# Kernel optimization log

Measured on AMD Instinct MI355X. Metric: run time of the kernel, lower is better.

The kernel has to match this reference:

```python
import jax, jax.numpy as jnp
import numpy as np

N_PTS = 262144
N_GAUSS = 2048
NZ, NY, NX = 100, 100, 100
MAX_SCALE = 0.02
BG = -1.0
CUTOFF = 9.0  # 3-sigma Mahalanobis cutoff
CHUNK = 1024


def quat_to_rot(q):
    # q: [G,4] normalized quaternion (r, x, y, z) as in 3DGS
    r, x, y, z = q[:, 0], q[:, 1], q[:, 2], q[:, 3]
    R = jnp.stack([
        1 - 2 * (y * y + z * z), 2 * (x * y - r * z), 2 * (x * z + r * y),
        2 * (x * y + r * z), 1 - 2 * (x * x + z * z), 2 * (y * z - r * x),
        2 * (x * z - r * y), 2 * (y * z + r * x), 1 - 2 * (x * x + y * y),
    ], axis=-1)
    return R.reshape(-1, 3, 3)


def setup_inputs() -> dict:
    key = jax.random.key(0)
    k = jax.random.split(key, 7)
    x = jax.random.uniform(k[0], (N_PTS, 3), jnp.float32, -1.0, 1.0)
    xyz = jax.random.uniform(k[1], (N_GAUSS, 3), jnp.float32)
    # raw log-scales so exp(raw) ~ 0.01 (Gaussians a few cells wide)
    scaling_raw = jax.random.normal(k[2], (N_GAUSS, 3), jnp.float32) * 0.3 + jnp.log(0.01)
    rotation_raw = jax.random.normal(k[3], (N_GAUSS, 4), jnp.float32)
    weight_raw = jax.random.normal(k[4], (N_GAUSS, 1), jnp.float32)
    values_raw = jax.random.normal(k[5], (N_GAUSS, 1), jnp.float32)
    valid_grid = jax.random.uniform(k[6], (NZ * NY * NX,)) < 0.8
    return {"x": x, "xyz": xyz, "scaling_raw": scaling_raw,
            "rotation_raw": rotation_raw, "weight_raw": weight_raw,
            "values_raw": values_raw, "valid_grid": valid_grid}


def _forward(x, xyz, scaling_raw, rotation_raw, weight_raw, values_raw, valid_grid):
    # valid-mask lookup from nearest grid cell
    x01 = (x + 1.0) * 0.5
    ix = jnp.clip(jnp.round(x01[:, 0] * (NX - 1)).astype(jnp.int32), 0, NX - 1)
    iy = jnp.clip(jnp.round(x01[:, 1] * (NY - 1)).astype(jnp.int32), 0, NY - 1)
    iz = jnp.clip(jnp.round(x01[:, 2] * (NZ - 1)).astype(jnp.int32), 0, NZ - 1)
    flat_idx = iz * (NY * NX) + iy * NX + ix
    valid = valid_grid[flat_idx]
    # world coords: mesh normalized to [0,1]^3 so vol_min=0, extent=1
    xw = x01
    # activations on Gaussian parameters
    s = jnp.exp(scaling_raw)
    r = jnp.linalg.norm(s, axis=1, keepdims=True) + 1e-8
    r_soft = MAX_SCALE * jnp.tanh(r / MAX_SCALE)
    s = s * (r_soft / r)                           # capped scales [G,3]
    qn = rotation_raw / jnp.maximum(
        jnp.linalg.norm(rotation_raw, axis=1, keepdims=True), 1e-12)
    R = quat_to_rot(qn)                            # [G,3,3]
    inv_s2 = 1.0 / (s * s)
    A = jnp.einsum('gik,gk,gjk->gij', R, inv_s2, R)  # inverse covariance [G,3,3]
    w = jax.nn.sigmoid(weight_raw[:, 0])           # [G]
    v = jax.nn.sigmoid(values_raw[:, 0])           # [G]
    wv = w * v
    xs = xw.reshape(-1, CHUNK, 3)                  # scan over point chunks

    def step(_, xc):
        d = xc[:, None, :] - xyz[None, :, :]       # [C,G,3]
        qd = jnp.einsum('cgi,gij,cgj->cg', d, A, d)
        g = jnp.where(qd <= CUTOFF, jnp.exp(-0.5 * qd), 0.0)  # [C,G]
        den = g @ w
        num = g @ wv
        y = jnp.where(den > 0, num / jnp.where(den > 0, den, 1.0), BG)
        return None, y

    _, ys = jax.lax.scan(step, None, xs)
    y = jnp.where(valid, ys.reshape(-1), 0.0)
    return y.reshape(-1, 1)


def reference(x, xyz, scaling_raw, rotation_raw, weight_raw, values_raw, valid_grid):
    return _forward(x, xyz, scaling_raw, rotation_raw, weight_raw, values_raw, valid_grid)
```

## Files before the change

kernel.cpp:

```cpp
#include <hip/hip_runtime.h>
#include <hip/hip_bf16.h>

namespace {

constexpr int GRIDC = 16;
constexpr int NCELL = GRIDC * GRIDC * GRIDC;
constexpr int CAP   = 48;
constexpr int RECF  = 16;
constexpr int PREPB = 8;
constexpr int CPB   = NCELL / PREPB;

__device__ __forceinline__ float sigmoid_(float v) {
    if (v >= 0.0f) { float e = expf(-v); return 1.0f / (1.0f + e); }
    float e = expf(v); return e / (1.0f + e);
}

__global__ void __launch_bounds__(256)
VEG_setup(const unsigned char* __restrict__ vg,
          const float* __restrict__ xyz, const float* __restrict__ sraw,
          const float* __restrict__ rraw, const float* __restrict__ wraw,
          const float* __restrict__ vraw,
          float* __restrict__ recs, int* __restrict__ counts,
          int* __restrict__ mode_p, int ng) {
    __shared__ int scount[CPB];
    __shared__ int sf1, sf3;
    if (threadIdx.x == 0) { sf1 = 0; sf3 = 0; }
    for (int c = threadIdx.x; c < CPB; c += 256) scount[c] = 0;
    __syncthreads();

    if (blockIdx.x == 0) {
        uint4 v = ((const uint4*)vg)[threadIdx.x];
        unsigned m = v.x | v.y | v.z | v.w;
        if (m & 0x0000FF00u) atomicOr(&sf1, 1);
        if (m & 0xFF000000u) atomicOr(&sf3, 1);
    }

    int cellbase = blockIdx.x * CPB;
    for (int g = threadIdx.x; g < ng; g += 256) {
        float s0 = expf(sraw[g * 3 + 0]);
        float s1 = expf(sraw[g * 3 + 1]);
        float s2 = expf(sraw[g * 3 + 2]);
        float r  = sqrtf(s0 * s0 + s1 * s1 + s2 * s2) + 1e-8f;
        float rs = 0.02f * tanhf(r / 0.02f);
        float fsc = rs / r;
        s0 *= fsc; s1 *= fsc; s2 *= fsc;

        float rad = 3.0f * fmaxf(fmaxf(s0, s1), s2);
        rad = rad * 1.001f + 1e-6f;
        float cx = xyz[g * 3 + 0], cy = xyz[g * 3 + 1], cz = xyz[g * 3 + 2];

        int xlo = max(0, (int)floorf((cx - rad) * (float)GRIDC));
        int xhi = min(GRIDC - 1, (int)floorf((cx + rad) * (float)GRIDC));
        int ylo = max(0, (int)floorf((cy - rad) * (float)GRIDC));
        int yhi = min(GRIDC - 1, (int)floorf((cy + rad) * (float)GRIDC));
        int zlo = max(0, (int)floorf((cz - rad) * (float)GRIDC));
        int zhi = min(GRIDC - 1, (int)floorf((cz + rad) * (float)GRIDC));
        int cmin = (zlo * GRIDC + ylo) * GRIDC + xlo;
        int cmax = (zhi * GRIDC + yhi) * GRIDC + xhi;
        if (cmax < cellbase || cmin >= cellbase + CPB) continue;

        float q0 = rraw[g * 4 + 0], q1 = rraw[g * 4 + 1];
        float q2 = rraw[g * 4 + 2], q3 = rraw[g * 4 + 3];
        float qn = fmaxf(sqrtf(q0 * q0 + q1 * q1 + q2 * q2 + q3 * q3), 1e-12f);
        float inv = 1.0f / qn;
        float rr = q0 * inv, qx = q1 * inv, qy = q2 * inv, qz = q3 * inv;
        float R00 = 1.0f - 2.0f * (qy * qy + qz * qz);
        float R01 = 2.0f * (qx * qy - rr * qz);
        float R02 = 2.0f * (qx * qz + rr * qy);
        float R10 = 2.0f * (qx * qy + rr * qz);
        float R11 = 1.0f - 2.0f * (qx * qx + qz * qz);
        float R12 = 2.0f * (qy * qz - rr * qx);
        float R20 = 2.0f * (qx * qz - rr * qy);
        float R21 = 2.0f * (qy * qz + rr * qx);
        float R22 = 1.0f - 2.0f * (qx * qx + qy * qy);

        float i0 = 1.0f / (s0 * s0), i1 = 1.0f / (s1 * s1), i2 = 1.0f / (s2 * s2);
        float4 rA = make_float4(cx, cy, cz,
                                R00 * R00 * i0 + R01 * R01 * i1 + R02 * R02 * i2);
        float4 rB = make_float4(R10 * R10 * i0 + R11 * R11 * i1 + R12 * R12 * i2,
                                R20 * R20 * i0 + R21 * R21 * i1 + R22 * R22 * i2,
                                R00 * R10 * i0 + R01 * R11 * i1 + R02 * R12 * i2,
                                R00 * R20 * i0 + R01 * R21 * i1 + R02 * R22 * i2);
        float w = sigmoid_(wraw[g]);
        float v = sigmoid_(vraw[g]);
        float4 rC = make_float4(R10 * R20 * i0 + R11 * R21 * i1 + R12 * R22 * i2,
                                w, w * v, 0.0f);

        for (int zz = zlo; zz <= zhi; ++zz)
            for (int yy = ylo; yy <= yhi; ++yy)
                for (int xx = xlo; xx <= xhi; ++xx) {
                    int cell  = (zz * GRIDC + yy) * GRIDC + xx;
                    int local = cell - cellbase;
                    if ((unsigned)local < (unsigned)CPB) {
                        int slot = atomicAdd(&scount[local], 1);
                        if (slot < CAP) {
                            float4* o = (float4*)(recs +
                                        ((size_t)cell * CAP + slot) * RECF);
                            o[0] = rA; o[1] = rB; o[2] = rC;
                        }
                    }
                }
    }
    __syncthreads();
    for (int c = threadIdx.x; c < CPB; c += 256) counts[cellbase + c] = scount[c];
    if (blockIdx.x == 0 && threadIdx.x == 0) *mode_p = sf1 ? 0 : (sf3 ? 2 : 1);
}

__global__ void __launch_bounds__(256)
VEG_splat(const float* __restrict__ x, const float* __restrict__ recs,
          const int* __restrict__ counts,
          const void* __restrict__ valid, const int* __restrict__ mode_p,
          float* __restrict__ out, int npts) {
    __shared__ float shx[768];
    int base = blockIdx.x * 256;
    int nrem = npts - base;
    if (nrem >= 256) {
        if (threadIdx.x < 192)
            ((float4*)shx)[threadIdx.x] = ((const float4*)(x + (size_t)base * 3))[threadIdx.x];
    } else {
        for (int j = threadIdx.x; j < nrem * 3; j += 256)
            shx[j] = x[(size_t)base * 3 + j];
    }
    __syncthreads();

    int i = base + threadIdx.x;
    if (i >= npts) return;

    float px = (shx[threadIdx.x * 3 + 0] + 1.0f) * 0.5f;
    float py = (shx[threadIdx.x * 3 + 1] + 1.0f) * 0.5f;
    float pz = (shx[threadIdx.x * 3 + 2] + 1.0f) * 0.5f;

    int cx = min(GRIDC - 1, (int)(px * (float)GRIDC));
    int cy = min(GRIDC - 1, (int)(py * (float)GRIDC));
    int cz = min(GRIDC - 1, (int)(pz * (float)GRIDC));
    int cell = (cz * GRIDC + cy) * GRIDC + cx;
    int cnt = counts[cell];
    const float4* rec = (const float4*)(recs + (size_t)cell * CAP * RECF);

    int ix = min(99, max(0, (int)rintf(px * 99.0f)));
    int iy = min(99, max(0, (int)rintf(py * 99.0f)));
    int iz = min(99, max(0, (int)rintf(pz * 99.0f)));
    int flat = iz * 10000 + iy * 100 + ix;

    int mode = *mode_p;
    bool vb;
    if (mode == 0)      vb = ((const unsigned char*)valid)[flat] != 0;
    else if (mode == 1) vb = ((const int*)valid)[flat] != 0;
    else                vb = ((const float*)valid)[flat] != 0.0f;

    cnt = (cnt < 0) ? 0 : min(cnt, CAP);
    float den = 0.0f, num = 0.0f;
#pragma unroll 2
    for (int j = 0; j < cnt; ++j) {
        float4 A = rec[j * 4 + 0], B = rec[j * 4 + 1], C = rec[j * 4 + 2];
        float dx = px - A.x, dy = py - A.y, dz = pz - A.z;
        float qd = A.w * dx * dx + B.x * dy * dy + B.y * dz * dz +
                   2.0f * (B.z * dx * dy + B.w * dx * dz + C.x * dy * dz);
        if (qd <= 9.0f) {
            float e = __expf(-0.5f * qd);
            den = fmaf(C.y, e, den);
            num = fmaf(C.z, e, num);
        }
    }
    float y = (den > 0.0f) ? (num / den) : -1.0f;
    out[i] = vb ? y : 0.0f;
}

__global__ void VEG_detect(const unsigned char* vg, int* mode) {
    __shared__ int f1, f3;
    if (threadIdx.x == 0) { f1 = 0; f3 = 0; }
    __syncthreads();
    for (int i = threadIdx.x; i < 4096; i += blockDim.x) {
        unsigned char b = vg[i];
        if (b) {
            int m = i & 3;
            if (m == 1) atomicOr(&f1, 1);
            if (m == 3) atomicOr(&f3, 1);
        }
    }
    __syncthreads();
    if (threadIdx.x == 0) *mode = f1 ? 0 : (f3 ? 2 : 1);
}

__global__ void __launch_bounds__(256)
VEG_brute(const float* __restrict__ x, const float* __restrict__ xyz,
          const float* __restrict__ sraw, const float* __restrict__ rraw,
          const float* __restrict__ wraw, const float* __restrict__ vraw,
          const void* __restrict__ valid, const int* __restrict__ mode_p,
          float* __restrict__ out, int npts, int ng) {
    __shared__ float sh[256 * 12];
    int i = blockIdx.x * blockDim.x + threadIdx.x;
    bool inb = i < npts;
    float px = 0, py = 0, pz = 0; int flat = 0;
    if (inb) {
        px = (x[i * 3 + 0] + 1.0f) * 0.5f;
        py = (x[i * 3 + 1] + 1.0f) * 0.5f;
        pz = (x[i * 3 + 2] + 1.0f) * 0.5f;
        int ix = min(99, max(0, (int)rintf(px * 99.0f)));
        int iy = min(99, max(0, (int)rintf(py * 99.0f)));
        int iz = min(99, max(0, (int)rintf(pz * 99.0f)));
        flat = iz * 10000 + iy * 100 + ix;
    }
    float den = 0.0f, num = 0.0f;
    for (int base = 0; base < ng; base += 256) {
        __syncthreads();
        int g = base + threadIdx.x;
        if (g < ng) {
            float s0 = expf(sraw[g * 3 + 0]);
            float s1 = expf(sraw[g * 3 + 1]);
            float s2 = expf(sraw[g * 3 + 2]);
            float r  = sqrtf(s0 * s0 + s1 * s1 + s2 * s2) + 1e-8f;
            float rs = 0.02f * tanhf(r / 0.02f);
            float fsc = rs / r;
            s0 *= fsc; s1 *= fsc; s2 *= fsc;
            float q0 = rraw[g * 4 + 0], q1 = rraw[g * 4 + 1];
            float q2 = rraw[g * 4 + 2], q3 = rraw[g * 4 + 3];
            float qn = fmaxf(sqrtf(q0 * q0 + q1 * q1 + q2 * q2 + q3 * q3), 1e-12f);
            float inv = 1.0f / qn;
            float rr = q0 * inv, qx = q1 * inv, qy = q2 * inv, qz = q3 * inv;
            float R00 = 1.0f - 2.0f * (qy * qy + qz * qz);
            float R01 = 2.0f * (qx * qy - rr * qz);
            float R02 = 2.0f * (qx * qz + rr * qy);
            float R10 = 2.0f * (qx * qy + rr * qz);
            float R11 = 1.0f - 2.0f * (qx * qx + qz * qz);
            float R12 = 2.0f * (qy * qz - rr * qx);
            float R20 = 2.0f * (qx * qz - rr * qy);
            float R21 = 2.0f * (qy * qz + rr * qx);
            float R22 = 1.0f - 2.0f * (qx * qx + qy * qy);
            float i0 = 1.0f / (s0 * s0), i1 = 1.0f / (s1 * s1), i2 = 1.0f / (s2 * s2);
            float* o = sh + threadIdx.x * 12;
            o[0] = xyz[g * 3 + 0]; o[1] = xyz[g * 3 + 1]; o[2] = xyz[g * 3 + 2];
            o[3] = R00 * R00 * i0 + R01 * R01 * i1 + R02 * R02 * i2;
            o[4] = R10 * R10 * i0 + R11 * R11 * i1 + R12 * R12 * i2;
            o[5] = R20 * R20 * i0 + R21 * R21 * i1 + R22 * R22 * i2;
            o[6] = R00 * R10 * i0 + R01 * R11 * i1 + R02 * R12 * i2;
            o[7] = R00 * R20 * i0 + R01 * R21 * i1 + R02 * R22 * i2;
            o[8] = R10 * R20 * i0 + R11 * R21 * i1 + R12 * R22 * i2;
            float w = sigmoid_(wraw[g]);
            float v = sigmoid_(vraw[g]);
            o[9] = w; o[10] = w * v; o[11] = 0.0f;
        }
        __syncthreads();
        int tile = min(256, ng - base);
        if (inb) {
            for (int j = 0; j < tile; ++j) {
                const float* o = sh + j * 12;
                float dx = px - o[0], dy = py - o[1], dz = pz - o[2];
                float qd = o[3] * dx * dx + o[4] * dy * dy + o[5] * dz * dz +
                           2.0f * (o[6] * dx * dy + o[7] * dx * dz + o[8] * dy * dz);
                if (qd <= 9.0f) {
                    float e = expf(-0.5f * qd);
                    den = fmaf(o[9], e, den);
                    num = fmaf(o[10], e, num);
                }
            }
        }
    }
    if (inb) {
        int mode = *mode_p;
        bool vb;
        if (mode == 0)      vb = ((const unsigned char*)valid)[flat] != 0;
        else if (mode == 1) vb = ((const int*)valid)[flat] != 0;
        else                vb = ((const float*)valid)[flat] != 0.0f;
        float y = (den > 0.0f) ? (num / den) : -1.0f;
        out[i] = vb ? y : 0.0f;
    }
}

}

extern "C" void kernel_launch(void* const* d_in, const int* in_sizes, int n_in,
                              void* d_out, int out_size, void* d_ws, size_t ws_size,
                              hipStream_t stream) {
    const float* x    = (const float*)d_in[0];
    const float* xyz  = (const float*)d_in[1];
    const float* sraw = (const float*)d_in[2];
    const float* rraw = (const float*)d_in[3];
    const float* wraw = (const float*)d_in[4];
    const float* vraw = (const float*)d_in[5];
    const void*  valid = d_in[6];
    float* out = (float*)d_out;

    int npts = in_sizes[0] / 3;
    int ng   = in_sizes[4];

    char* ws = (char*)d_ws;
    size_t mode_off   = 0;
    size_t counts_off = 256;
    size_t recs_off   = counts_off + (size_t)NCELL * sizeof(int);
    recs_off = (recs_off + 255) & ~(size_t)255;
    size_t total = recs_off + (size_t)NCELL * CAP * RECF * sizeof(float);

    int* mode = (int*)(ws + mode_off);

    if (ws_size >= total) {
        int*   counts = (int*)(ws + counts_off);
        float* recs   = (float*)(ws + recs_off);
        VEG_setup<<<PREPB, 256, 0, stream>>>((const unsigned char*)valid, xyz, sraw,
                                             rraw, wraw, vraw, recs, counts, mode, ng);
        VEG_splat<<<(npts + 255) / 256, 256, 0, stream>>>(x, recs, counts,
                                                          valid, mode, out, npts);
    } else {
        VEG_detect<<<1, 256, 0, stream>>>((const unsigned char*)valid, mode);
        VEG_brute<<<(npts + 255) / 256, 256, 0, stream>>>(x, xyz, sraw, rraw, wraw,
                                                          vraw, valid, mode, out,
                                                          npts, ng);
    }
}
```

Baseline: 120.1 us.

## Store per-Gaussian params once and bin cells by index lists

After: 112.2 us. 6.5% less time.

```diff
diff --git a/kernel.cpp b/kernel.cpp
--- a/kernel.cpp
+++ b/kernel.cpp
@@ -6,7 +6,6 @@
 constexpr int GRIDC = 16;
 constexpr int NCELL = GRIDC * GRIDC * GRIDC;
 constexpr int CAP   = 48;
-constexpr int RECF  = 16;
 constexpr int PREPB = 8;
 constexpr int CPB   = NCELL / PREPB;
 
@@ -20,8 +19,8 @@
           const float* __restrict__ xyz, const float* __restrict__ sraw,
           const float* __restrict__ rraw, const float* __restrict__ wraw,
           const float* __restrict__ vraw,
-          float* __restrict__ recs, int* __restrict__ counts,
-          int* __restrict__ mode_p, int ng) {
+          float* __restrict__ gdata, int* __restrict__ lists,
+          int* __restrict__ counts, int* __restrict__ mode_p, int ng) {
     __shared__ int scount[CPB];
     __shared__ int sf1, sf3;
     if (threadIdx.x == 0) { sf1 = 0; sf3 = 0; }
@@ -35,32 +34,18 @@
         if (m & 0xFF000000u) atomicOr(&sf3, 1);
     }
 
-    int cellbase = blockIdx.x * CPB;
-    for (int g = threadIdx.x; g < ng; g += 256) {
-        float s0 = expf(sraw[g * 3 + 0]);
-        float s1 = expf(sraw[g * 3 + 1]);
-        float s2 = expf(sraw[g * 3 + 2]);
+    int g0 = blockIdx.x * 256 + threadIdx.x;
+    if (g0 < ng) {
+        float s0 = expf(sraw[g0 * 3 + 0]);
+        float s1 = expf(sraw[g0 * 3 + 1]);
+        float s2 = expf(sraw[g0 * 3 + 2]);
         float r  = sqrtf(s0 * s0 + s1 * s1 + s2 * s2) + 1e-8f;
         float rs = 0.02f * tanhf(r / 0.02f);
         float fsc = rs / r;
         s0 *= fsc; s1 *= fsc; s2 *= fsc;
 
-        float rad = 3.0f * fmaxf(fmaxf(s0, s1), s2);
-        rad = rad * 1.001f + 1e-6f;
-        float cx = xyz[g * 3 + 0], cy = xyz[g * 3 + 1], cz = xyz[g * 3 + 2];
-
-        int xlo = max(0, (int)floorf((cx - rad) * (float)GRIDC));
-        int xhi = min(GRIDC - 1, (int)floorf((cx + rad) * (float)GRIDC));
-        int ylo = max(0, (int)floorf((cy - rad) * (float)GRIDC));
-        int yhi = min(GRIDC - 1, (int)floorf((cy + rad) * (float)GRIDC));
-        int zlo = max(0, (int)floorf((cz - rad) * (float)GRIDC));
-        int zhi = min(GRIDC - 1, (int)floorf((cz + rad) * (float)GRIDC));
-        int cmin = (zlo * GRIDC + ylo) * GRIDC + xlo;
-        int cmax = (zhi * GRIDC + yhi) * GRIDC + xhi;
-        if (cmax < cellbase || cmin >= cellbase + CPB) continue;
-
-        float q0 = rraw[g * 4 + 0], q1 = rraw[g * 4 + 1];
-        float q2 = rraw[g * 4 + 2], q3 = rraw[g * 4 + 3];
+        float q0 = rraw[g0 * 4 + 0], q1 = rraw[g0 * 4 + 1];
+        float q2 = rraw[g0 * 4 + 2], q3 = rraw[g0 * 4 + 3];
         float qn = fmaxf(sqrtf(q0 * q0 + q1 * q1 + q2 * q2 + q3 * q3), 1e-12f);
         float inv = 1.0f / qn;
         float rr = q0 * inv, qx = q1 * inv, qy = q2 * inv, qz = q3 * inv;
@@ -75,16 +60,48 @@
         float R22 = 1.0f - 2.0f * (qx * qx + qy * qy);
 
         float i0 = 1.0f / (s0 * s0), i1 = 1.0f / (s1 * s1), i2 = 1.0f / (s2 * s2);
-        float4 rA = make_float4(cx, cy, cz,
-                                R00 * R00 * i0 + R01 * R01 * i1 + R02 * R02 * i2);
-        float4 rB = make_float4(R10 * R10 * i0 + R11 * R11 * i1 + R12 * R12 * i2,
-                                R20 * R20 * i0 + R21 * R21 * i1 + R22 * R22 * i2,
-                                R00 * R10 * i0 + R01 * R11 * i1 + R02 * R12 * i2,
-                                R00 * R20 * i0 + R01 * R21 * i1 + R02 * R22 * i2);
-        float w = sigmoid_(wraw[g]);
-        float v = sigmoid_(vraw[g]);
-        float4 rC = make_float4(R10 * R20 * i0 + R11 * R21 * i1 + R12 * R22 * i2,
-                                w, w * v, 0.0f);
+        float w = sigmoid_(wraw[g0]);
+        float v = sigmoid_(vraw[g0]);
+        float rad = 3.0f * fmaxf(fmaxf(s0, s1), s2);
+        rad = rad * 1.001f + 1e-6f;
+
+        float* o = gdata + (size_t)g0 * 12;
+        o[0]  = xyz[g0 * 3 + 0];
+        o[1]  = xyz[g0 * 3 + 1];
+        o[2]  = xyz[g0 * 3 + 2];
+        o[3]  = R00 * R00 * i0 + R01 * R01 * i1 + R02 * R02 * i2;
+        o[4]  = R10 * R10 * i0 + R11 * R11 * i1 + R12 * R12 * i2;
+        o[5]  = R20 * R20 * i0 + R21 * R21 * i1 + R22 * R22 * i2;
+        o[6]  = R00 * R10 * i0 + R01 * R11 * i1 + R02 * R12 * i2;
+        o[7]  = R00 * R20 * i0 + R01 * R21 * i1 + R02 * R22 * i2;
+        o[8]  = R10 * R20 * i0 + R11 * R21 * i1 + R12 * R22 * i2;
+        o[9]  = w;
+        o[10] = w * v;
+        o[11] = rad;
+    }
+
+    int cellbase = blockIdx.x * CPB;
+    for (int g = threadIdx.x; g < ng; g += 256) {
+        float s0 = expf(sraw[g * 3 + 0]);
+        float s1 = expf(sraw[g * 3 + 1]);
+        float s2 = expf(sraw[g * 3 + 2]);
+        float r  = sqrtf(s0 * s0 + s1 * s1 + s2 * s2) + 1e-8f;
+        float rs = 0.02f * tanhf(r / 0.02f);
+        float fsc = rs / r;
+        s0 *= fsc; s1 *= fsc; s2 *= fsc;
+        float rad = 3.0f * fmaxf(fmaxf(s0, s1), s2);
+        rad = rad * 1.001f + 1e-6f;
+
+        float cx = xyz[g * 3 + 0], cy = xyz[g * 3 + 1], cz = xyz[g * 3 + 2];
+        int xlo = max(0, (int)floorf((cx - rad) * (float)GRIDC));
+        int xhi = min(GRIDC - 1, (int)floorf((cx + rad) * (float)GRIDC));
+        int ylo = max(0, (int)floorf((cy - rad) * (float)GRIDC));
+        int yhi = min(GRIDC - 1, (int)floorf((cy + rad) * (float)GRIDC));
+        int zlo = max(0, (int)floorf((cz - rad) * (float)GRIDC));
+        int zhi = min(GRIDC - 1, (int)floorf((cz + rad) * (float)GRIDC));
+        int cmin = (zlo * GRIDC + ylo) * GRIDC + xlo;
+        int cmax = (zhi * GRIDC + yhi) * GRIDC + xhi;
+        if (cmax < cellbase || cmin >= cellbase + CPB) continue;
 
         for (int zz = zlo; zz <= zhi; ++zz)
             for (int yy = ylo; yy <= yhi; ++yy)
@@ -93,11 +110,7 @@
                     int local = cell - cellbase;
                     if ((unsigned)local < (unsigned)CPB) {
                         int slot = atomicAdd(&scount[local], 1);
-                        if (slot < CAP) {
-                            float4* o = (float4*)(recs +
-                                        ((size_t)cell * CAP + slot) * RECF);
-                            o[0] = rA; o[1] = rB; o[2] = rC;
-                        }
+                        if (slot < CAP) lists[cell * CAP + slot] = g;
                     }
                 }
     }
@@ -107,8 +120,8 @@
 }
 
 __global__ void __launch_bounds__(256)
-VEG_splat(const float* __restrict__ x, const float* __restrict__ recs,
-          const int* __restrict__ counts,
+VEG_splat(const float* __restrict__ x, const float* __restrict__ gdata,
+          const int* __restrict__ lists, const int* __restrict__ counts,
           const void* __restrict__ valid, const int* __restrict__ mode_p,
           float* __restrict__ out, int npts) {
     __shared__ float shx[768];
@@ -135,7 +148,7 @@
     int cz = min(GRIDC - 1, (int)(pz * (float)GRIDC));
     int cell = (cz * GRIDC + cy) * GRIDC + cx;
     int cnt = counts[cell];
-    const float4* rec = (const float4*)(recs + (size_t)cell * CAP * RECF);
+    const int* lst = lists + cell * CAP;
 
     int ix = min(99, max(0, (int)rintf(px * 99.0f)));
     int iy = min(99, max(0, (int)rintf(py * 99.0f)));
@@ -152,7 +165,9 @@
     float den = 0.0f, num = 0.0f;
 #pragma unroll 2
     for (int j = 0; j < cnt; ++j) {
-        float4 A = rec[j * 4 + 0], B = rec[j * 4 + 1], C = rec[j * 4 + 2];
+        int g = lst[j];
+        const float4* gd = (const float4*)(gdata + (size_t)g * 12);
+        float4 A = gd[0], B = gd[1], C = gd[2];
         float dx = px - A.x, dy = py - A.y, dz = pz - A.z;
         float qd = A.w * dx * dx + B.x * dy * dy + B.y * dz * dz +
                    2.0f * (B.z * dx * dy + B.w * dx * dz + C.x * dy * dz);
@@ -287,18 +302,22 @@
     char* ws = (char*)d_ws;
     size_t mode_off   = 0;
     size_t counts_off = 256;
-    size_t recs_off   = counts_off + (size_t)NCELL * sizeof(int);
-    recs_off = (recs_off + 255) & ~(size_t)255;
-    size_t total = recs_off + (size_t)NCELL * CAP * RECF * sizeof(float);
+    size_t gdata_off  = counts_off + (size_t)NCELL * sizeof(int);
+    gdata_off = (gdata_off + 255) & ~(size_t)255;
+    size_t lists_off  = gdata_off + (size_t)ng * 12 * sizeof(float);
+    lists_off = (lists_off + 255) & ~(size_t)255;
+    size_t total = lists_off + (size_t)NCELL * CAP * sizeof(int);
 
     int* mode = (int*)(ws + mode_off);
 
-    if (ws_size >= total) {
+    if (ws_size >= total && ng <= PREPB * 256) {
         int*   counts = (int*)(ws + counts_off);
-        float* recs   = (float*)(ws + recs_off);
+        float* gdata  = (float*)(ws + gdata_off);
+        int*   lists  = (int*)(ws + lists_off);
         VEG_setup<<<PREPB, 256, 0, stream>>>((const unsigned char*)valid, xyz, sraw,
-                                             rraw, wraw, vraw, recs, counts, mode, ng);
-        VEG_splat<<<(npts + 255) / 256, 256, 0, stream>>>(x, recs, counts,
+                                             rraw, wraw, vraw, gdata, lists, counts,
+                                             mode, ng);
+        VEG_splat<<<(npts + 255) / 256, 256, 0, stream>>>(x, gdata, lists, counts,
                                                           valid, mode, out, npts);
     } else {
         VEG_detect<<<1, 256, 0, stream>>>((const unsigned char*)valid, mode);
```
